# Performance work log

Measured on AMD Instinct MI355X. Metric: run time of the kernel, lower is better.

Reference implementation:

```python
import jax, jax.numpy as jnp
import numpy as np

K = 12          # tagset size incl START/STOP
START = 10
STOP = 11
NEG = -10000.0
B, T, V, D, H = 64, 1024, 50000, 256, 512
Hh = H // 2


def setup_inputs() -> dict:
    key = jax.random.key(0)
    ks = jax.random.split(key, 20)
    sentence = jax.random.randint(ks[0], (B, T), 1, V)
    seq_lens = jax.random.randint(ks[1], (B,), T // 2, T + 1)
    emb = jax.random.normal(ks[2], (V, D), dtype=jnp.float32) * 0.1
    emb = emb.at[0].set(0.0)  # padding_idx=0
    s = 1.0 / np.sqrt(Hh)

    def u(k, shape):
        return jax.random.uniform(k, shape, minval=-s, maxval=s, dtype=jnp.float32)

    Wih_f = u(ks[3], (4 * Hh, D)); Whh_f = u(ks[4], (4 * Hh, Hh))
    bih_f = u(ks[5], (4 * Hh,));  bhh_f = u(ks[6], (4 * Hh,))
    Wih_b = u(ks[7], (4 * Hh, D)); Whh_b = u(ks[8], (4 * Hh, Hh))
    bih_b = u(ks[9], (4 * Hh,));  bhh_b = u(ks[10], (4 * Hh,))
    sl = 1.0 / np.sqrt(H)
    Wtag = jax.random.uniform(ks[11], (K, H), minval=-sl, maxval=sl, dtype=jnp.float32)
    btag = jax.random.uniform(ks[12], (K,), minval=-sl, maxval=sl, dtype=jnp.float32)
    transitions = jax.random.normal(ks[13], (K, K), dtype=jnp.float32)
    transitions = transitions.at[START, :].set(NEG).at[:, STOP].set(NEG)
    h0 = jax.random.normal(ks[14], (2, B, Hh), dtype=jnp.float32)
    c0 = jax.random.normal(ks[15], (2, B, Hh), dtype=jnp.float32)
    return dict(sentence=sentence, seq_lens=seq_lens, emb=emb,
                Wih_f=Wih_f, Whh_f=Whh_f, bih_f=bih_f, bhh_f=bhh_f,
                Wih_b=Wih_b, Whh_b=Whh_b, bih_b=bih_b, bhh_b=bhh_b,
                Wtag=Wtag, btag=btag, transitions=transitions, h0=h0, c0=c0)


def _lstm_dir(x, mask, h0, c0, Wih, Whh, bih, bhh, reverse):
    # x: [B,T,D], mask: [B,T] bool. Masked steps keep the carried state
    # (equivalent to PyTorch packed-sequence semantics for positions < seq_len).
    def step(carry, inp):
        h, c = carry
        xt, mt = inp  # [B,D], [B,1]
        z = xt @ Wih.T + h @ Whh.T + bih + bhh  # [B,4Hh], torch gate order i,f,g,o
        i, f, g, o = jnp.split(z, 4, axis=-1)
        c2 = jax.nn.sigmoid(f) * c + jax.nn.sigmoid(i) * jnp.tanh(g)
        h2 = jax.nn.sigmoid(o) * jnp.tanh(c2)
        h = jnp.where(mt, h2, h)
        c = jnp.where(mt, c2, c)
        return (h, c), h
    xs = (x.transpose(1, 0, 2), mask.T[:, :, None])
    _, hs = jax.lax.scan(step, (h0, c0), xs, reverse=reverse)
    return hs.transpose(1, 0, 2)  # [B,T,Hh]


def reference(sentence, seq_lens, emb, Wih_f, Whh_f, bih_f, bhh_f,
              Wih_b, Whh_b, bih_b, bhh_b, Wtag, btag, transitions, h0, c0):
    Bn, Tn = sentence.shape
    mask = jnp.arange(Tn)[None, :] < seq_lens[:, None]  # [B,T]
    x = emb[sentence]  # [B,T,D]
    hf = _lstm_dir(x, mask, h0[0], c0[0], Wih_f, Whh_f, bih_f, bhh_f, False)
    hb = _lstm_dir(x, mask, h0[1], c0[1], Wih_b, Whh_b, bih_b, bhh_b, True)
    feats = jnp.concatenate([hf, hb], -1) @ Wtag.T + btag  # [B,T,K]

    # Vectorized Viterbi over batch and tags (replaces per-tag python loops)
    fv0 = jnp.full((Bn, K), NEG, dtype=feats.dtype).at[:, START].set(0.0)
    ident = jnp.arange(K)[None, :]

    def vstep(fv, inp):
        ft, mt = inp  # [B,K], [B]
        sc = fv[:, None, :] + transitions[None, :, :]  # [B,Knext,Kprev]
        bp = jnp.argmax(sc, -1)                        # [B,K]
        vmax = jnp.max(sc, -1) + ft
        fv2 = jnp.where(mt[:, None], vmax, fv)
        bp = jnp.where(mt[:, None], bp, ident)         # identity passthrough on pad
        return fv2, bp

    fv, bptrs = jax.lax.scan(vstep, fv0, (feats.transpose(1, 0, 2), mask.T))
    term = fv + transitions[STOP][None, :]
    best = jnp.argmax(term, -1)   # [B]
    score = jnp.max(term, -1)     # [B]

    def btrace(tag, bp):
        prev = jnp.take_along_axis(bp, tag[:, None], 1)[:, 0]
        return prev, tag

    _, path = jax.lax.scan(btrace, best, bptrs, reverse=True)  # [T,B]
    path = jnp.where(mask, path.T, 0)  # [B,T], zeros beyond seq_len
    return score, path
```

## Files before the change

### kernel.cpp

```cpp
#include <hip/hip_runtime.h>
#include <math.h>

#define NEG10K -10000.0f

static const size_t OFF_WT_IH = 0;
static const size_t OFF_WT_HH = 524288;
static const size_t OFF_BIAS  = 1048576;
static const size_t OFF_WTAGD = 1050624;
static const size_t OFF_BTAG  = 1058816;
static const size_t OFF_FEATS = 1058832;
static const size_t OFF_HC    = 3155984;
static const size_t OFF_CC    = 3188752;
static const size_t OFF_PUB   = 3221520;
static const size_t OFF_G     = 3352592;

__device__ __forceinline__ float sigf(float x) { return 1.0f / (1.0f + expf(-x)); }

__global__ __launch_bounds__(256) void k_transpose(
    const float* __restrict__ wih_f, const float* __restrict__ wih_b,
    const float* __restrict__ whh_f, const float* __restrict__ whh_b,
    float* __restrict__ ws) {
  __shared__ float tile[32][33];
  int z = blockIdx.z;
  const float* src = (z == 0) ? wih_f : (z == 1) ? wih_b : (z == 2) ? whh_f : whh_b;
  float* dst = ws + ((z < 2) ? (OFF_WT_IH + (size_t)z * 262144)
                             : (OFF_WT_HH + (size_t)(z - 2) * 262144));
  int r0 = blockIdx.y * 32;
  int c0 = blockIdx.x * 32;
  int tid = threadIdx.x;
  int c = tid & 31, rg = tid >> 5;
#pragma unroll
  for (int i = 0; i < 4; ++i) {
    int r = rg * 4 + i;
    tile[r][c] = src[(size_t)(r0 + r) * 256 + c0 + c];
  }
  __syncthreads();
  int r2 = tid & 31, cg = tid >> 5;
#pragma unroll
  for (int i = 0; i < 4; ++i) {
    int ccv = cg * 4 + i;
    dst[(size_t)(c0 + ccv) * 1024 + r0 + r2] = tile[r2][ccv];
  }
}

__global__ __launch_bounds__(256) void k_prep_small(
    const float* __restrict__ bih_f, const float* __restrict__ bhh_f,
    const float* __restrict__ bih_b, const float* __restrict__ bhh_b,
    const float* __restrict__ wtag, const float* __restrict__ btag,
    float* __restrict__ ws) {
  int i = blockIdx.x * 256 + threadIdx.x;
  if (i < 2048) {
    int d = i >> 10, n = i & 1023;
    ws[OFF_BIAS + i] = d ? (bih_b[n] + bhh_b[n]) : (bih_f[n] + bhh_f[n]);
  } else if (i < 2048 + 8192) {
    int r = i - 2048;
    int d = r >> 12, rem = r & 4095;
    int k = rem >> 8, j = rem & 255;
    ws[OFF_WTAGD + r] = (k < 12) ? wtag[(size_t)k * 512 + d * 256 + j] : 0.0f;
  } else if (i < 2048 + 8192 + 16) {
    int kk = i - 10240;
    ws[OFF_BTAG + kk] = (kk < 12) ? btag[kk] : 0.0f;
  } else if (i < 10256 + 131072) {
    ws[OFF_PUB + (i - 10256)] = 0.0f;
  }
}

__global__ __launch_bounds__(256) void k_gemm_g(
    const int* __restrict__ sentence, const float* __restrict__ emb,
    const float* __restrict__ ws_c, float* __restrict__ G,
    int t0, int cshift) {
  __shared__ float As[32][64];
  __shared__ float Bs[32][64];
  __shared__ int idx_s[64];
  int d = blockIdx.z;
  int m0 = blockIdx.y * 64, n0 = blockIdx.x * 64;
  int tid = threadIdx.x;
  int cmask = (1 << cshift) - 1;
  const float* Wt = ws_c + OFF_WT_IH + (size_t)d * 262144;
  if (tid < 64) {
    int m = m0 + tid;
    int b = m >> cshift, tt = m & cmask;
    int t = d ? (1023 - t0 - tt) : (t0 + tt);
    idx_s[tid] = sentence[(size_t)b * 1024 + t];
  }
  __syncthreads();
  float acc[4][4] = {};
  int tm = tid >> 4, tn = tid & 15;
  int am = tid & 63, ak = (tid >> 6) * 8;
  int bn = (tid & 15) * 4, bk = tid >> 4;
  for (int k0 = 0; k0 < 256; k0 += 32) {
    const float* ar = emb + (size_t)idx_s[am] * 256 + k0 + ak;
    float4 a0 = *(const float4*)ar;
    float4 a1 = *(const float4*)(ar + 4);
    float4 b0 = *(const float4*)(Wt + (size_t)(k0 + bk) * 1024 + n0 + bn);
    float4 b1 = *(const float4*)(Wt + (size_t)(k0 + bk + 16) * 1024 + n0 + bn);
    As[ak + 0][am] = a0.x; As[ak + 1][am] = a0.y; As[ak + 2][am] = a0.z; As[ak + 3][am] = a0.w;
    As[ak + 4][am] = a1.x; As[ak + 5][am] = a1.y; As[ak + 6][am] = a1.z; As[ak + 7][am] = a1.w;
    *(float4*)&Bs[bk][bn] = b0;
    *(float4*)&Bs[bk + 16][bn] = b1;
    __syncthreads();
#pragma unroll
    for (int kk = 0; kk < 32; ++kk) {
      float4 av = *(const float4*)&As[kk][tm * 4];
      float4 bv = *(const float4*)&Bs[kk][tn * 4];
      float avf[4] = {av.x, av.y, av.z, av.w};
      float bvf[4] = {bv.x, bv.y, bv.z, bv.w};
#pragma unroll
      for (int i = 0; i < 4; ++i)
#pragma unroll
        for (int j = 0; j < 4; ++j) acc[i][j] = fmaf(avf[i], bvf[j], acc[i][j]);
    }
    __syncthreads();
  }
  float4 bias = *(const float4*)(ws_c + OFF_BIAS + (size_t)d * 1024 + n0 + tn * 4);
#pragma unroll
  for (int i = 0; i < 4; ++i) {
    int m = m0 + tm * 4 + i;
    int b = m >> cshift, tt = m & cmask;
    float* gp = G + (((size_t)d * 64 + b) * (size_t)(cmask + 1) + tt) * 1024 + n0 + tn * 4;
    float4 v;
    v.x = acc[i][0] + bias.x; v.y = acc[i][1] + bias.y;
    v.z = acc[i][2] + bias.z; v.w = acc[i][3] + bias.w;
    *(float4*)gp = v;
  }
}

#define FMA4(A, W, S) { A.x = fmaf(W.x, S, A.x); A.y = fmaf(W.y, S, A.y); \
                        A.z = fmaf(W.z, S, A.z); A.w = fmaf(W.w, S, A.w); }
__global__ __launch_bounds__(512) void k_lstm_split(
    const float* __restrict__ ws_c, const float* __restrict__ G,
    const float* __restrict__ h0p, const float* __restrict__ c0p,
    const int* __restrict__ seq_lens, float* __restrict__ ws_mut,
    int t0, int chunkT, int first) {
  __shared__ float zpart[8][4][128];
  __shared__ float zs[4][128];
  __shared__ float h_s[4][256];
  __shared__ float ldspad[16384];

  int bx = blockIdx.x;
  int w   = (bx >> 3) & 7;
  int gid = (bx & 7) + ((bx >> 6) << 3);
  int d   = gid >> 4;
  int bq4 = (gid & 15) * 4;
  int u0  = w * 32;
  int tid = threadIdx.x;
  if (first == 777) {
    ldspad[tid] = (float)tid; __syncthreads(); zs[0][0] = ldspad[tid ^ 1];
  }

  int cg = tid & 31, kq = tid >> 5;
  int c4 = cg * 4;
  int wv = tid >> 6, ln = tid & 63;

  const float* WhhT = ws_c + OFF_WT_HH + (size_t)d * 262144;
  int wcol = (cg >> 3) * 256 + u0 + (cg & 7) * 4;
  float4 wr[16];
#pragma unroll
  for (int i = 0; i < 16; ++i)
    wr[i] = *(const float4*)(WhhT + (size_t)(kq * 16 + i) * 1024 + wcol);

  const float* hsrc = first ? h0p : (ws_c + OFF_HC);
  for (int i = tid; i < 1024; i += 512) {
    int b = i >> 8, u = i & 255;
    h_s[b][u] = hsrc[((size_t)d * 64 + bq4 + b) * 256 + u];
  }
  float cc = 0.0f; int mylen = 0;
  int ob = tid >> 5, ou = tid & 31;
  if (tid < 128) {
    const float* csrc = first ? c0p : (ws_c + OFF_CC);
    cc = csrc[((size_t)d * 64 + bq4 + ob) * 256 + u0 + ou];
    mylen = seq_lens[bq4 + ob];
  }
  int tb_b = wv >> 1;
  int tb_k = (wv & 1) * 8 + (ln >> 3);
  int tb_j = ln & 7;
  float wtag_r[32];
  {
    const float* wtg = ws_c + OFF_WTAGD + (size_t)d * 4096 + tb_k * 256;
#pragma unroll
    for (int i = 0; i < 32; ++i) wtag_r[i] = wtg[tb_j + 8 * i];
  }
  unsigned long long* pub64 = (unsigned long long*)(ws_mut + OFF_PUB);
  float* featsD = ws_mut + OFF_FEATS + (size_t)d * 1048576;
  int bB = tid >> 7, jB = tid & 127;
  bool bail = false;
  __syncthreads();

  for (int s = 0; s < chunkT; ++s) {
    int gs = t0 + s;
    int t = d ? (1023 - gs) : gs;
    int p = gs & 1;
    unsigned tag = (unsigned)(gs + 1);
    float gval = G[(((size_t)d * 64 + bq4 + bB) * (size_t)chunkT + s) * 1024 +
                   (jB >> 5) * 256 + u0 + (jB & 31)];
    float4 acc[4] = {{0,0,0,0},{0,0,0,0},{0,0,0,0},{0,0,0,0}};
#pragma unroll
    for (int i = 0; i < 4; ++i) {
      int k = kq * 16 + i * 4;
      float4 w0 = wr[i * 4], w1 = wr[i * 4 + 1], w2 = wr[i * 4 + 2], w3 = wr[i * 4 + 3];
#pragma unroll
      for (int b = 0; b < 4; ++b) {
        float4 hv = *(const float4*)&h_s[b][k];
        FMA4(acc[b], w0, hv.x); FMA4(acc[b], w1, hv.y);
        FMA4(acc[b], w2, hv.z); FMA4(acc[b], w3, hv.w);
      }
    }
#pragma unroll
    for (int b = 0; b < 4; ++b) {
      acc[b].x += __shfl_xor(acc[b].x, 32);
      acc[b].y += __shfl_xor(acc[b].y, 32);
      acc[b].z += __shfl_xor(acc[b].z, 32);
      acc[b].w += __shfl_xor(acc[b].w, 32);
    }
    if ((tid & 32) == 0) {
#pragma unroll
      for (int b = 0; b < 4; ++b) *(float4*)&zpart[wv][b][c4] = acc[b];
    }
    __syncthreads();
    zs[bB][jB] = zpart[0][bB][jB] + zpart[1][bB][jB] + zpart[2][bB][jB] + zpart[3][bB][jB] +
                 zpart[4][bB][jB] + zpart[5][bB][jB] + zpart[6][bB][jB] + zpart[7][bB][jB] + gval;
    __syncthreads();
    if (tid < 128) {
      float zi = zs[ob][ou], zf = zs[ob][32 + ou], zg = zs[ob][64 + ou], zo = zs[ob][96 + ou];
      float cn = sigf(zf) * cc + sigf(zi) * tanhf(zg);
      float hn = sigf(zo) * tanhf(cn);
      bool m = t < mylen;
      cc = m ? cn : cc;
      float hp = m ? hn : h_s[ob][u0 + ou];
      union { float f; unsigned u; } hb; hb.f = hp;
      unsigned long long pk = ((unsigned long long)tag << 32) | (unsigned long long)hb.u;
      __hip_atomic_store(
          pub64 + (size_t)p * 32768 + ((size_t)d * 64 + bq4 + ob) * 256 + (u0 + ou),
          pk, __ATOMIC_RELAXED, __HIP_MEMORY_SCOPE_AGENT);
    }
    if (s > 0) {
      int tp = d ? (1023 - (gs - 1)) : (gs - 1);
      float pv = 0.0f;
#pragma unroll
      for (int i = 0; i < 32; ++i)
        pv = fmaf(h_s[tb_b][tb_j + 8 * i], wtag_r[i], pv);
      pv += __shfl_xor(pv, 1);
      pv += __shfl_xor(pv, 2);
      pv += __shfl_xor(pv, 4);
      if (w == 0 && tb_j == 0)
        featsD[(size_t)(bq4 + tb_b) * 16384 + (size_t)tp * 16 + tb_k] = pv;
    }
    __syncthreads();
    for (int e = tid; e < 1024; e += 512) {
      int b = e >> 8, u = e & 255;
      size_t idx = (size_t)p * 32768 + ((size_t)d * 64 + bq4 + b) * 256 + u;
      unsigned long long v =
          __hip_atomic_load(pub64 + idx, __ATOMIC_RELAXED, __HIP_MEMORY_SCOPE_AGENT);
      unsigned spin = 0;
      while ((unsigned)(v >> 32) != tag && !bail) {
        __builtin_amdgcn_s_sleep(1);
        v = __hip_atomic_load(pub64 + idx, __ATOMIC_RELAXED, __HIP_MEMORY_SCOPE_AGENT);
        if (++spin > 2000000u) { bail = true; break; }
      }
      union { unsigned u32; float f; } cv; cv.u32 = (unsigned)v;
      h_s[b][u] = cv.f;
    }
    __syncthreads();
  }
  {
    int tl = d ? (1023 - (t0 + chunkT - 1)) : (t0 + chunkT - 1);
    float pv = 0.0f;
#pragma unroll
    for (int i = 0; i < 32; ++i)
      pv = fmaf(h_s[tb_b][tb_j + 8 * i], wtag_r[i], pv);
    pv += __shfl_xor(pv, 1);
    pv += __shfl_xor(pv, 2);
    pv += __shfl_xor(pv, 4);
    if (w == 0 && tb_j == 0)
      featsD[(size_t)(bq4 + tb_b) * 16384 + (size_t)tl * 16 + tb_k] = pv;
  }
  if (tid < 128)
    ws_mut[OFF_CC + ((size_t)d * 64 + bq4 + ob) * 256 + u0 + ou] = cc;
  if (w == 0)
    for (int i = tid; i < 1024; i += 512)
      ws_mut[OFF_HC + ((size_t)d * 64 + bq4 + (i >> 8)) * 256 + (i & 255)] = h_s[i >> 8][i & 255];
}

__global__ __launch_bounds__(256) void k_lstm_fused(
    const float* __restrict__ ws_c, const int* __restrict__ sentence,
    const float* __restrict__ emb, const float* __restrict__ h0p,
    const float* __restrict__ c0p, const int* __restrict__ seq_lens,
    float* __restrict__ ws_mut) {
  int d = blockIdx.x & 1;
  int pr = blockIdx.x >> 1;
  int b0 = pr * 2, b1 = b0 + 1;
  const float* Wih = ws_c + OFF_WT_IH + (size_t)d * 262144;
  const float* Whh = ws_c + OFF_WT_HH + (size_t)d * 262144;
  __shared__ float h_s[2][256];
  __shared__ float x_s[2][2][256];
  __shared__ float z_s[2][1024];
  __shared__ int   sent_s[2][1024];
  __shared__ float wt_s[16][260];
  __shared__ float pfp_s[2][16][8];
  int tid = threadIdx.x;
  int len0 = seq_lens[b0], len1 = seq_lens[b1];
  for (int i = tid; i < 2048; i += 256)
    sent_s[i >> 10][i & 1023] = sentence[(size_t)(b0 + (i >> 10)) * 1024 + (i & 1023)];
  for (int i = tid; i < 4096; i += 256)
    wt_s[i >> 8][i & 255] = ws_c[OFF_WTAGD + (size_t)d * 4096 + i];
  h_s[0][tid] = h0p[((size_t)d * 64 + b0) * 256 + tid];
  h_s[1][tid] = h0p[((size_t)d * 64 + b1) * 256 + tid];
  float cc0 = c0p[((size_t)d * 64 + b0) * 256 + tid];
  float cc1 = c0p[((size_t)d * 64 + b1) * 256 + tid];
  int c4 = tid * 4;
  float4 bias_v = *(const float4*)(ws_c + OFF_BIAS + (size_t)d * 1024 + c4);
  __syncthreads();
  int t0 = d ? 1023 : 0;
  if (tid < 128) {
    int bb = tid >> 6, l = tid & 63;
    int row = sent_s[bb][t0];
    *(float4*)&x_s[0][bb][l * 4] = *(const float4*)(emb + (size_t)row * 256 + l * 4);
  }
  __syncthreads();
  float* featsD = ws_mut + OFF_FEATS + (size_t)d * 1048576;
  for (int s = 0; s < 1024; ++s) {
    int t = d ? (1023 - s) : s;
    int cur = s & 1, nxt = cur ^ 1;
    float4 pf = {0, 0, 0, 0};
    if (tid < 128) {
      int sn = (s < 1023) ? (s + 1) : 1023;
      int tn = d ? (1023 - sn) : sn;
      int bb = tid >> 6, l = tid & 63;
      pf = *(const float4*)(emb + (size_t)sent_s[bb][tn] * 256 + l * 4);
    }
    float4 a0 = bias_v, a1 = bias_v;
#pragma unroll 4
    for (int k = 0; k < 256; k += 4) {
      float4 xv0 = *(const float4*)&x_s[cur][0][k];
      float4 xv1 = *(const float4*)&x_s[cur][1][k];
      float4 hv0 = *(const float4*)&h_s[0][k];
      float4 hv1 = *(const float4*)&h_s[1][k];
      const float* wi = Wih + (size_t)k * 1024 + c4;
      const float* wh = Whh + (size_t)k * 1024 + c4;
      float4 wi0 = *(const float4*)(wi);
      float4 wi1 = *(const float4*)(wi + 1024);
      float4 wi2 = *(const float4*)(wi + 2048);
      float4 wi3 = *(const float4*)(wi + 3072);
      float4 wh0 = *(const float4*)(wh);
      float4 wh1 = *(const float4*)(wh + 1024);
      float4 wh2 = *(const float4*)(wh + 2048);
      float4 wh3 = *(const float4*)(wh + 3072);
      FMA4(a0, wi0, xv0.x); FMA4(a0, wi1, xv0.y); FMA4(a0, wi2, xv0.z); FMA4(a0, wi3, xv0.w);
      FMA4(a0, wh0, hv0.x); FMA4(a0, wh1, hv0.y); FMA4(a0, wh2, hv0.z); FMA4(a0, wh3, hv0.w);
      FMA4(a1, wi0, xv1.x); FMA4(a1, wi1, xv1.y); FMA4(a1, wi2, xv1.z); FMA4(a1, wi3, xv1.w);
      FMA4(a1, wh0, hv1.x); FMA4(a1, wh1, hv1.y); FMA4(a1, wh2, hv1.z); FMA4(a1, wh3, hv1.w);
    }
    *(float4*)&z_s[0][c4] = a0;
    *(float4*)&z_s[1][c4] = a1;
    __syncthreads();
    {
      float iv = z_s[0][tid], fv = z_s[0][tid + 256];
      float gv = z_s[0][tid + 512], ov = z_s[0][tid + 768];
      float cn = sigf(fv) * cc0 + sigf(iv) * tanhf(gv);
      float hn = sigf(ov) * tanhf(cn);
      bool m = t < len0;
      cc0 = m ? cn : cc0;
      h_s[0][tid] = m ? hn : h_s[0][tid];
    }
    {
      float iv = z_s[1][tid], fv = z_s[1][tid + 256];
      float gv = z_s[1][tid + 512], ov = z_s[1][tid + 768];
      float cn = sigf(fv) * cc1 + sigf(iv) * tanhf(gv);
      float hn = sigf(ov) * tanhf(cn);
      bool m = t < len1;
      cc1 = m ? cn : cc1;
      h_s[1][tid] = m ? hn : h_s[1][tid];
    }
    if (tid < 128) {
      int bb = tid >> 6, l = tid & 63;
      *(float4*)&x_s[nxt][bb][l * 4] = pf;
    }
    __syncthreads();
    {
      int b2 = tid >> 7, r = tid & 127;
      int ks = r >> 3, jg = r & 7;
      const float* hv = &h_s[b2][jg * 32];
      const float* wv = &wt_s[ks][jg * 32];
      float p = 0.0f;
#pragma unroll
      for (int i = 0; i < 32; ++i) p = fmaf(hv[i], wv[i], p);
      pfp_s[b2][ks][jg] = p;
    }
    __syncthreads();
    if (tid < 32) {
      int b = tid >> 4, k = tid & 15;
      float sum = 0.0f;
#pragma unroll
      for (int i = 0; i < 8; ++i) sum += pfp_s[b][k][i];
      featsD[(size_t)(b0 + b) * 16384 + (size_t)t * 16 + k] = sum;
    }
  }
}

__global__ __launch_bounds__(64) void k_viterbi(const float* __restrict__ ws_c,
                                                const float* __restrict__ trans,
                                                const int* __restrict__ seq_lens,
                                                float* __restrict__ out) {
  __shared__ char bp_s[1024][12];
  int b = blockIdx.x, lane = threadIdx.x;
  int len = seq_lens[b];
  float trow[12];
#pragma unroll
  for (int p = 0; p < 12; ++p) trow[p] = (lane < 12) ? trans[lane * 12 + p] : 0.0f;
  float tb = (lane < 16) ? ws_c[OFF_BTAG + lane] : 0.0f;
  float fv = (lane == 10) ? 0.0f : NEG10K;
  const float* ff = ws_c + OFF_FEATS + (size_t)b * 16384;
  const float* fb = ws_c + OFF_FEATS + 1048576 + (size_t)b * 16384;
  for (int t = 0; t < 1024; ++t) {
    float ft = (lane < 16) ? (ff[t * 16 + lane] + fb[t * 16 + lane] + tb) : 0.0f;
    float best = -3.0e38f; int arg = 0;
#pragma unroll
    for (int p = 0; p < 12; ++p) {
      float s = __shfl(fv, p) + trow[p];
      if (s > best) { best = s; arg = p; }
    }
    bool m = t < len;
    if (m) fv = best + ft;
    if (lane < 12) bp_s[t][lane] = (char)(m ? arg : lane);
  }
  float term = (lane < 12) ? fv + trans[132 + lane] : -3.0e38f;
  float bestv = -3.0e38f; int bestp = 0;
#pragma unroll
  for (int p = 0; p < 12; ++p) {
    float v = __shfl(term, p);
    if (v > bestv) { bestv = v; bestp = p; }
  }
  __syncthreads();
  if (lane == 0) {
    out[b] = bestv;
    int tag = bestp;
    float* po = out + 64 + (size_t)b * 1024;
    for (int t = 1023; t >= 0; --t) {
      po[t] = (t < len) ? (float)tag : 0.0f;
      tag = bp_s[t][tag];
    }
  }
}

extern "C" void kernel_launch(void* const* d_in, const int* in_sizes, int n_in,
                              void* d_out, int out_size, void* d_ws, size_t ws_size,
                              hipStream_t stream) {
  (void)in_sizes; (void)n_in; (void)out_size;
  const int*   sentence = (const int*)d_in[0];
  const int*   seq_lens = (const int*)d_in[1];
  const float* emb      = (const float*)d_in[2];
  const float* wih_f    = (const float*)d_in[3];
  const float* whh_f    = (const float*)d_in[4];
  const float* bih_f    = (const float*)d_in[5];
  const float* bhh_f    = (const float*)d_in[6];
  const float* wih_b    = (const float*)d_in[7];
  const float* whh_b    = (const float*)d_in[8];
  const float* bih_b    = (const float*)d_in[9];
  const float* bhh_b    = (const float*)d_in[10];
  const float* wtag     = (const float*)d_in[11];
  const float* btag     = (const float*)d_in[12];
  const float* trans    = (const float*)d_in[13];
  const float* h0p      = (const float*)d_in[14];
  const float* c0p      = (const float*)d_in[15];
  float* ws  = (float*)d_ws;
  float* out = (float*)d_out;
  size_t avail = ws_size / 4;
  if (avail < OFF_FEATS + 2097152) return;

  int chunkT = 0;
  const int opts[5] = {512, 256, 128, 64, 32};
  for (int i = 0; i < 5; ++i)
    if (OFF_G + (size_t)131072 * opts[i] <= avail) { chunkT = opts[i]; break; }

  k_transpose<<<dim3(8, 32, 4), 256, 0, stream>>>(wih_f, wih_b, whh_f, whh_b, ws);
  k_prep_small<<<553, 256, 0, stream>>>(bih_f, bhh_f, bih_b, bhh_b, wtag, btag, ws);
  if (chunkT) {
    int cshift = 31 - __builtin_clz(chunkT);
    int nc = 1024 / chunkT;
    for (int c = 0; c < nc; ++c) {
      int t0 = c * chunkT;
      k_gemm_g<<<dim3(16, chunkT, 2), 256, 0, stream>>>(sentence, emb, ws, ws + OFF_G,
                                                        t0, cshift);
      k_lstm_split<<<256, 512, 0, stream>>>(ws, ws + OFF_G, h0p, c0p, seq_lens, ws,
                                            t0, chunkT, c == 0);
    }
  } else {
    k_lstm_fused<<<64, 256, 0, stream>>>(ws, sentence, emb, h0p, c0p, seq_lens, ws);
  }
  k_viterbi<<<64, 64, 0, stream>>>(ws, trans, seq_lens, out);
}
```

Measured before the change: 4.468 ms.

## Double-buffer hidden state and drop barriers in split LSTM recurrence step

Double-buffers the shared hidden-state array so the gather of the next step's h no longer needs a barrier before it. This removes two of the four __syncthreads per step. The gate reduction is now done directly by the 128 owner threads, each summing the eight partials, so the intermediate zs buffer and its barrier go away. The precomputed input-gate values G are prefetched into registers one step ahead, and each thread polls two published elements concurrently. The trade is more per-owner reduction work and extra shared memory for the second h buffer.

```diff
diff --git a/kernel.cpp b/kernel.cpp
--- a/kernel.cpp
+++ b/kernel.cpp
@@ -133,8 +133,7 @@
     const int* __restrict__ seq_lens, float* __restrict__ ws_mut,
     int t0, int chunkT, int first) {
   __shared__ float zpart[8][4][128];
-  __shared__ float zs[4][128];
-  __shared__ float h_s[4][256];
+  __shared__ float h_s[2][4][256];
   __shared__ float ldspad[16384];
 
   int bx = blockIdx.x;
@@ -145,7 +144,7 @@
   int u0  = w * 32;
   int tid = threadIdx.x;
   if (first == 777) {
-    ldspad[tid] = (float)tid; __syncthreads(); zs[0][0] = ldspad[tid ^ 1];
+    ldspad[tid] = (float)tid; __syncthreads(); zpart[0][0][0] = ldspad[tid ^ 1];
   }
 
   int cg = tid & 31, kq = tid >> 5;
@@ -162,14 +161,18 @@
   const float* hsrc = first ? h0p : (ws_c + OFF_HC);
   for (int i = tid; i < 1024; i += 512) {
     int b = i >> 8, u = i & 255;
-    h_s[b][u] = hsrc[((size_t)d * 64 + bq4 + b) * 256 + u];
+    h_s[0][b][u] = hsrc[((size_t)d * 64 + bq4 + b) * 256 + u];
   }
   float cc = 0.0f; int mylen = 0;
   int ob = tid >> 5, ou = tid & 31;
-  if (tid < 128) {
+  bool owner = tid < 128;
+  const float* Gown = G + (((size_t)d * 64 + bq4 + ob) * (size_t)chunkT) * 1024 + u0 + ou;
+  float gv0 = 0, gv1 = 0, gv2 = 0, gv3 = 0;
+  if (owner) {
     const float* csrc = first ? c0p : (ws_c + OFF_CC);
     cc = csrc[((size_t)d * 64 + bq4 + ob) * 256 + u0 + ou];
     mylen = seq_lens[bq4 + ob];
+    gv0 = Gown[0]; gv1 = Gown[256]; gv2 = Gown[512]; gv3 = Gown[768];
   }
   int tb_b = wv >> 1;
   int tb_k = (wv & 1) * 8 + (ln >> 3);
@@ -182,8 +185,10 @@
   }
   unsigned long long* pub64 = (unsigned long long*)(ws_mut + OFF_PUB);
   float* featsD = ws_mut + OFF_FEATS + (size_t)d * 1048576;
-  int bB = tid >> 7, jB = tid & 127;
+  int gb0 = tid >> 8, gu0 = tid & 255;
+  int gb1 = 2 + (tid >> 8), gu1 = tid & 255;
   bool bail = false;
+  int hcur = 0;
   __syncthreads();
 
   for (int s = 0; s < chunkT; ++s) {
@@ -191,8 +196,8 @@
     int t = d ? (1023 - gs) : gs;
     int p = gs & 1;
     unsigned tag = (unsigned)(gs + 1);
-    float gval = G[(((size_t)d * 64 + bq4 + bB) * (size_t)chunkT + s) * 1024 +
-                   (jB >> 5) * 256 + u0 + (jB & 31)];
+    float (*hc)[256] = h_s[hcur];
+    float (*hn)[256] = h_s[hcur ^ 1];
     float4 acc[4] = {{0,0,0,0},{0,0,0,0},{0,0,0,0},{0,0,0,0}};
 #pragma unroll
     for (int i = 0; i < 4; ++i) {
@@ -200,7 +205,7 @@
       float4 w0 = wr[i * 4], w1 = wr[i * 4 + 1], w2 = wr[i * 4 + 2], w3 = wr[i * 4 + 3];
 #pragma unroll
       for (int b = 0; b < 4; ++b) {
-        float4 hv = *(const float4*)&h_s[b][k];
+        float4 hv = *(const float4*)&hc[b][k];
         FMA4(acc[b], w0, hv.x); FMA4(acc[b], w1, hv.y);
         FMA4(acc[b], w2, hv.z); FMA4(acc[b], w3, hv.w);
       }
@@ -217,16 +222,25 @@
       for (int b = 0; b < 4; ++b) *(float4*)&zpart[wv][b][c4] = acc[b];
     }
     __syncthreads();
-    zs[bB][jB] = zpart[0][bB][jB] + zpart[1][bB][jB] + zpart[2][bB][jB] + zpart[3][bB][jB] +
-                 zpart[4][bB][jB] + zpart[5][bB][jB] + zpart[6][bB][jB] + zpart[7][bB][jB] + gval;
-    __syncthreads();
-    if (tid < 128) {
-      float zi = zs[ob][ou], zf = zs[ob][32 + ou], zg = zs[ob][64 + ou], zo = zs[ob][96 + ou];
+    if (owner) {
+      float f0 = zpart[0][ob][ou],       f1 = zpart[0][ob][32 + ou];
+      float f2 = zpart[0][ob][64 + ou],  f3 = zpart[0][ob][96 + ou];
+#pragma unroll
+      for (int w2 = 1; w2 < 8; ++w2) {
+        f0 += zpart[w2][ob][ou];       f1 += zpart[w2][ob][32 + ou];
+        f2 += zpart[w2][ob][64 + ou];  f3 += zpart[w2][ob][96 + ou];
+      }
+      float zi = f0 + gv0, zf = f1 + gv1, zg = f2 + gv2, zo = f3 + gv3;
+      {
+        int sn = (s + 1 < chunkT) ? (s + 1) : s;
+        const float* gp = Gown + (size_t)sn * 1024;
+        gv0 = gp[0]; gv1 = gp[256]; gv2 = gp[512]; gv3 = gp[768];
+      }
       float cn = sigf(zf) * cc + sigf(zi) * tanhf(zg);
-      float hn = sigf(zo) * tanhf(cn);
+      float hn2 = sigf(zo) * tanhf(cn);
       bool m = t < mylen;
       cc = m ? cn : cc;
-      float hp = m ? hn : h_s[ob][u0 + ou];
+      float hp = m ? hn2 : hc[ob][u0 + ou];
       union { float f; unsigned u; } hb; hb.f = hp;
       unsigned long long pk = ((unsigned long long)tag << 32) | (unsigned long long)hb.u;
       __hip_atomic_store(
@@ -238,47 +252,56 @@
       float pv = 0.0f;
 #pragma unroll
       for (int i = 0; i < 32; ++i)
-        pv = fmaf(h_s[tb_b][tb_j + 8 * i], wtag_r[i], pv);
+        pv = fmaf(hc[tb_b][tb_j + 8 * i], wtag_r[i], pv);
       pv += __shfl_xor(pv, 1);
       pv += __shfl_xor(pv, 2);
       pv += __shfl_xor(pv, 4);
       if (w == 0 && tb_j == 0)
         featsD[(size_t)(bq4 + tb_b) * 16384 + (size_t)tp * 16 + tb_k] = pv;
     }
-    __syncthreads();
-    for (int e = tid; e < 1024; e += 512) {
-      int b = e >> 8, u = e & 255;
-      size_t idx = (size_t)p * 32768 + ((size_t)d * 64 + bq4 + b) * 256 + u;
-      unsigned long long v =
-          __hip_atomic_load(pub64 + idx, __ATOMIC_RELAXED, __HIP_MEMORY_SCOPE_AGENT);
+    {
+      size_t base = (size_t)p * 32768 + ((size_t)d * 64 + bq4) * 256;
+      size_t i0 = base + (size_t)gb0 * 256 + gu0;
+      size_t i1 = base + (size_t)gb1 * 256 + gu1;
+      unsigned long long v0 =
+          __hip_atomic_load(pub64 + i0, __ATOMIC_RELAXED, __HIP_MEMORY_SCOPE_AGENT);
+      unsigned long long v1 =
+          __hip_atomic_load(pub64 + i1, __ATOMIC_RELAXED, __HIP_MEMORY_SCOPE_AGENT);
       unsigned spin = 0;
-      while ((unsigned)(v >> 32) != tag && !bail) {
+      while ((((unsigned)(v0 >> 32) != tag) || ((unsigned)(v1 >> 32) != tag)) && !bail) {
         __builtin_amdgcn_s_sleep(1);
-        v = __hip_atomic_load(pub64 + idx, __ATOMIC_RELAXED, __HIP_MEMORY_SCOPE_AGENT);
+        if ((unsigned)(v0 >> 32) != tag)
+          v0 = __hip_atomic_load(pub64 + i0, __ATOMIC_RELAXED, __HIP_MEMORY_SCOPE_AGENT);
+        if ((unsigned)(v1 >> 32) != tag)
+          v1 = __hip_atomic_load(pub64 + i1, __ATOMIC_RELAXED, __HIP_MEMORY_SCOPE_AGENT);
         if (++spin > 2000000u) { bail = true; break; }
       }
-      union { unsigned u32; float f; } cv; cv.u32 = (unsigned)v;
-      h_s[b][u] = cv.f;
-    }
-    __syncthreads();
+      union { unsigned u32; float f; } cv0, cv1;
+      cv0.u32 = (unsigned)v0; cv1.u32 = (unsigned)v1;
+      hn[gb0][gu0] = cv0.f;
+      hn[gb1][gu1] = cv1.f;
+    }
+    __syncthreads();
+    hcur ^= 1;
   }
   {
+    float (*hc)[256] = h_s[hcur];
     int tl = d ? (1023 - (t0 + chunkT - 1)) : (t0 + chunkT - 1);
     float pv = 0.0f;
 #pragma unroll
     for (int i = 0; i < 32; ++i)
-      pv = fmaf(h_s[tb_b][tb_j + 8 * i], wtag_r[i], pv);
+      pv = fmaf(hc[tb_b][tb_j + 8 * i], wtag_r[i], pv);
     pv += __shfl_xor(pv, 1);
     pv += __shfl_xor(pv, 2);
     pv += __shfl_xor(pv, 4);
     if (w == 0 && tb_j == 0)
       featsD[(size_t)(bq4 + tb_b) * 16384 + (size_t)tl * 16 + tb_k] = pv;
-  }
-  if (tid < 128)
-    ws_mut[OFF_CC + ((size_t)d * 64 + bq4 + ob) * 256 + u0 + ou] = cc;
-  if (w == 0)
-    for (int i = tid; i < 1024; i += 512)
-      ws_mut[OFF_HC + ((size_t)d * 64 + bq4 + (i >> 8)) * 256 + (i & 255)] = h_s[i >> 8][i & 255];
+    if (owner)
+      ws_mut[OFF_CC + ((size_t)d * 64 + bq4 + ob) * 256 + u0 + ou] = cc;
+    if (w == 0)
+      for (int i = tid; i < 1024; i += 512)
+        ws_mut[OFF_HC + ((size_t)d * 64 + bq4 + (i >> 8)) * 256 + (i & 255)] = hc[i >> 8][i & 255];
+  }
 }
 
 __global__ __launch_bounds__(256) void k_lstm_fused(
```

New measurement: 5.024 ms. 1.12x slower.
